# Optimization experiments

Hardware: AMD Instinct MI355X
Metric: run time of the kernel (lower is better)

The kernel has to match this reference:

```python
import jax, jax.numpy as jnp
import numpy as np

B, N, T, D, M, HOPS = 32, 300, 12, 64, 16, 2

def setup_inputs() -> dict:
    key = jax.random.key(0)
    ks = jax.random.split(key, 12)
    inp = {
        "X": jax.random.normal(ks[0], (B, D, N, T), dtype=jnp.float32),
        "timeEmbedding": jax.random.normal(ks[1], (B, N, T, D), dtype=jnp.float32),
        "adjW": jax.random.normal(ks[2], (N, D), dtype=jnp.float32) * (1.0 / np.sqrt(D)),
        "adjB": jnp.zeros((N,), dtype=jnp.float32),
        "trainW1": jax.random.normal(ks[3], (N, M), dtype=jnp.float32) * 0.1,
        "trainW2": jax.random.normal(ks[4], (M, D * D), dtype=jnp.float32) * 0.1,
        "alpha1": jax.random.normal(ks[5], (N, M), dtype=jnp.float32) * 0.1,
        "alpha2": jax.random.normal(ks[6], (M, N), dtype=jnp.float32) * 0.1,
        "beta1": jax.random.normal(ks[7], (N, M), dtype=jnp.float32) * 0.1,
        "beta2": jax.random.normal(ks[8], (M, N), dtype=jnp.float32) * 0.1,
        "gcnW": jax.random.normal(ks[9], (D, D * (HOPS + 1)), dtype=jnp.float32) * (1.0 / np.sqrt(D * (HOPS + 1))),
        "gcnB": jnp.zeros((D,), dtype=jnp.float32),
    }
    return inp

def reference(X, timeEmbedding, adjW, adjB, trainW1, trainW2, alpha1, alpha2, beta1, beta2, gcnW, gcnB):
    # timeEmbedding: [B,N,T,D] -> [B,T,N,D]
    te = jnp.transpose(timeEmbedding, (0, 2, 1, 3))
    # learned adjacency: A[b,t,n,k]
    A = jnp.sin(jnp.einsum('btnd,kd->btnk', te, adjW) + adjB)  # Linear(dmodel->N)
    A = (alpha1 @ alpha2) * A            # elementwise scale by [N,N], broadcast over b,t
    A = jax.nn.relu(A + beta1 @ beta2)
    # X: [B,D,N,T] -> [B,T,N,D]
    Xp = jnp.transpose(X, (0, 3, 2, 1))
    # per-node weight matrices [N,D,D]
    W = (trainW1 @ trainW2).reshape(N, D, D)
    Hs = [Xp]
    Hb = Xp
    for _ in range(HOPS):
        Hnow = jnp.einsum('btnk,btkd->btnd', A, Hb)      # adjacency aggregation
        Hnow = jnp.einsum('btnk,nkd->btnd', Hnow, W)     # per-node distinct matmul
        pre = Xp + Hnow
        Hnow = jax.nn.sigmoid(pre) * jnp.tanh(pre)        # gated residual
        Hs.append(Hnow)
        Hb = Hnow
    H = jnp.concatenate(Hs, axis=3)                       # [B,T,N,D*(hops+1)]
    Hout = jnp.einsum('btnf,df->btnd', H, gcnW) + gcnB    # gcnLinear (dropout = identity in eval)
    return jnp.transpose(Hout, (0, 3, 2, 1))              # [B,D,N,T]
```

## Files before the change

kernel.cpp:

```cpp
#include <hip/hip_runtime.h>

#define Nq 300
#define Tq 12
#define Dq 64
#define Mq 16
#define BTq 384
#define DDq (Dq*Dq)
#define Fq (Dq*3)
#define NP 320

typedef short bf8_t __attribute__((ext_vector_type(8)));
typedef float f4_t  __attribute__((ext_vector_type(4)));

__device__ __forceinline__ unsigned short f2bf(float f) {
    unsigned u = __float_as_uint(f);
    u = (u + 0x7FFFu + ((u >> 16) & 1u)) >> 16;
    return (unsigned short)u;
}
__device__ __forceinline__ float bf2f(unsigned short u) {
    return __uint_as_float((unsigned)u << 16);
}
__device__ __forceinline__ unsigned cvtpk(float lo, float hi) {
    unsigned r;
    asm("v_cvt_pk_bf16_f32 %0, %1, %2" : "=v"(r) : "v"(lo), "v"(hi));
    return r;
}
__device__ __forceinline__ float4 ld4(const float* p) { return *(const float4*)p; }

__device__ __forceinline__ bf8_t pack8(float4 a, float4 b) {
    union { unsigned u[4]; bf8_t v; } q;
    q.u[0] = cvtpk(a.x, a.y); q.u[1] = cvtpk(a.z, a.w);
    q.u[2] = cvtpk(b.x, b.y); q.u[3] = cvtpk(b.z, b.w);
    return q.v;
}

__device__ __forceinline__ float gatef(float p) {
    float pc = fminf(fmaxf(p, -30.f), 30.f);
    float u = __expf(pc);
    return u * (u - 1.f) / (u * u + 1.f);
}

__global__ void __launch_bounds__(256) kprep_all(
    const float* __restrict__ a1, const float* __restrict__ a2,
    const float* __restrict__ b1, const float* __restrict__ b2,
    const float* __restrict__ w1, const float* __restrict__ w2,
    const float* __restrict__ adjW, const float* __restrict__ adjB,
    const float* __restrict__ X,
    unsigned* __restrict__ ABt, unsigned short* __restrict__ Wt,
    unsigned short* __restrict__ adjWb, float* __restrict__ adjBp,
    unsigned short* __restrict__ Xp_t, unsigned short* __restrict__ Xp_nb)
{
    __shared__ char smem[64 * 308 * 2];
    const int vb = blockIdx.x;
    const int tid = threadIdx.x;

    if (vb < 400) {
        const int tile = vb;
        const int reg = tid & 3, lane = tid >> 2;
        const int nt = tile % 5;  int r1 = tile / 5;
        const int w  = r1 % 4;    int r2 = r1 / 4;
        const int c  = r2 % 5;    const int qi = r2 / 5;
        const int n = qi*80 + nt*16 + (lane & 15);
        const int k = c*64 + w*16 + (lane >> 4)*4 + reg;
        unsigned outv = 0u;
        if (n < Nq && k < Nq) {
            float sa = 0.f, sb = 0.f;
            #pragma unroll
            for (int m = 0; m < Mq; ++m) {
                sa = fmaf(a1[n*Mq+m], a2[m*Nq+k], sa);
                sb = fmaf(b1[n*Mq+m], b2[m*Nq+k], sb);
            }
            outv = cvtpk(sa, sb);
        }
        ABt[tile*256 + tid] = outv;
    } else if (vb < 700) {
        float* sT = (float*)smem;
        __shared__ float sw1[Mq];
        const int n = vb - 400;
        if (tid < Mq) sw1[tid] = w1[n*Mq + tid];
        __syncthreads();
        for (int i = tid; i < DDq; i += 256) {
            int k = i >> 6, d = i & 63;
            float s = 0.f;
            #pragma unroll
            for (int m = 0; m < Mq; ++m) s = fmaf(sw1[m], w2[m*DDq + i], s);
            sT[d*65 + k] = s;
        }
        __syncthreads();
        for (int i = tid; i < DDq; i += 256) {
            int d = i >> 6, k = i & 63;
            Wt[(size_t)n*DDq + i] = f2bf(sT[d*65 + k]);
        }
    } else if (vb < 780) {
        int e = (vb - 700) * 256 + tid;
        if (e < NP * 64) {
            int k = e >> 6, d = e & 63;
            adjWb[e] = (k < Nq) ? f2bf(adjW[k*Dq + d]) : (unsigned short)0;
        }
        if (e < NP) adjBp[e] = (e < Nq) ? adjB[e] : 0.f;
    } else {
        unsigned short* sT = (unsigned short*)smem;
        const int bx = vb - 780;
        const int b = bx / 24, sub = bx % 24;
        const int tile = sub >> 1, half = sub & 1;
        const int n0 = tile * 25, d0 = half * 32;
        for (int i = tid; i < 32 * 75; i += 256) {
            int dl = i / 75, jq = i - dl*75, j = jq*4;
            float4 v = ld4(&X[(size_t)(b*64 + d0 + dl)*3600 + n0*12 + j]);
            *(uint2*)&sT[dl*308 + j] = make_uint2(cvtpk(v.x, v.y), cvtpk(v.z, v.w));
        }
        __syncthreads();
        for (int wi = tid; wi < 12 * 32 * 25; wi += 256) {
            int nl = wi % 25, rem = wi / 25;
            int dl = rem & 31, t = rem >> 5;
            Xp_t[((size_t)(b*Tq + t)*64 + d0 + dl)*NP + n0 + nl] = sT[dl*308 + nl*12 + t];
        }
        if (tile == 11) {
            for (int wi = tid; wi < 12 * 32 * 20; wi += 256) {
                int e = wi % 20, rem = wi / 20;
                int dl = rem & 31, t = rem >> 5;
                Xp_t[((size_t)(b*Tq + t)*64 + d0 + dl)*NP + 300 + e] = 0;
            }
        }
        for (int wi = tid; wi < 25 * 12 * 8; wi += 256) {
            int dg = wi & 7, rem = wi >> 3;
            int t = rem % 12, nl = rem / 12;
            ushort4 o;
            o.x = sT[(dg*4+0)*308 + nl*12 + t];
            o.y = sT[(dg*4+1)*308 + nl*12 + t];
            o.z = sT[(dg*4+2)*308 + nl*12 + t];
            o.w = sT[(dg*4+3)*308 + nl*12 + t];
            *(ushort4*)&Xp_nb[((size_t)(n0+nl)*BTq + b*Tq + t)*64 + d0 + dg*4] = o;
        }
    }
}

__global__ void __launch_bounds__(256) ktr2(const unsigned short* __restrict__ Hnb,
                                            unsigned short* __restrict__ Ht) {
    __shared__ unsigned short sT[64 * 308];
    const int bt = blockIdx.x;
    const int tid = threadIdx.x;
    for (int i = tid; i < 300 * 8; i += 256) {
        int nl = i >> 3, dg = i & 7;
        bf8_t v = *(const bf8_t*)&Hnb[((size_t)nl*BTq + bt)*64 + dg*8];
        #pragma unroll
        for (int k = 0; k < 8; ++k)
            sT[(dg*8+k)*308 + nl] = (unsigned short)v[k];
    }
    __syncthreads();
    for (int wi = tid; wi < 64 * 80; wi += 256) {
        int kq = wi % 80, d = wi / 80;
        ushort4 o;
        int k = kq * 4;
        o.x = (k+0 < Nq) ? sT[d*308 + k+0] : (unsigned short)0;
        o.y = (k+1 < Nq) ? sT[d*308 + k+1] : (unsigned short)0;
        o.z = (k+2 < Nq) ? sT[d*308 + k+2] : (unsigned short)0;
        o.w = (k+3 < Nq) ? sT[d*308 + k+3] : (unsigned short)0;
        *(ushort4*)&Ht[((size_t)bt*64 + d)*NP + k] = o;
    }
}

template<int HOP>
__global__ void __launch_bounds__(256) kfuse_t(
    const float* __restrict__ te,
    unsigned short* __restrict__ teP,
    const unsigned short* __restrict__ adjWb,
    const float* __restrict__ adjBp,
    const unsigned* __restrict__ ABt,
    const unsigned short* __restrict__ Hb_t,
    unsigned short* __restrict__ Hout_nb)
{
    __shared__ unsigned short sP[80 * 72];
    __shared__ unsigned short sT[80 * 68];
    const int bt = blockIdx.x >> 2, qi = blockIdx.x & 3;
    const int b = bt / Tq, t = bt - b * Tq;
    const int nbase = qi * 80;
    const int tid = threadIdx.x;
    const int w = tid >> 6, lane = tid & 63, quad = lane >> 4, l16 = lane & 15;
    const int dcol = w*16 + l16;
    const int nrows = (Nq - nbase < 80) ? (Nq - nbase) : 80;

    if (HOP == 1) {
        #pragma unroll
        for (int r = 0; r < 5; ++r) {
            int row = r*16 + (tid >> 4);
            int col = (tid & 15) * 4;
            int n = nbase + row; if (n > Nq-1) n = Nq-1;
            float4 v = ld4(te + (((size_t)b*Nq + n)*Tq + t)*Dq + col);
            *(uint2*)&sT[row*68 + col] = make_uint2(cvtpk(v.x, v.y), cvtpk(v.z, v.w));
        }
    } else {
        for (int idx = tid; idx < 80*8; idx += 256) {
            int row = idx >> 3, cg = idx & 7;
            int n = nbase + row; if (n > Nq-1) n = Nq-1;
            *(bf8_t*)&sT[row*68 + cg*8] =
                *(const bf8_t*)&teP[((size_t)bt*Nq + n)*64 + cg*8];
        }
    }
    __syncthreads();
    if (HOP == 1) {
        for (int idx = tid; idx < nrows*8; idx += 256) {
            int row = idx >> 3, cg = idx & 7;
            *(bf8_t*)&teP[((size_t)bt*Nq + nbase + row)*64 + cg*8] =
                *(const bf8_t*)&sT[row*68 + cg*8];
        }
    }
    bf8_t tb0[5], tb1[5];
    #pragma unroll
    for (int nt = 0; nt < 5; ++nt) {
        const unsigned short* tr = &sT[(nt*16 + l16)*68];
        tb0[nt] = *(const bf8_t*)(tr + quad*8);
        tb1[nt] = *(const bf8_t*)(tr + 32 + quad*8);
    }

    f4_t accO[5];
    #pragma unroll
    for (int rt = 0; rt < 5; ++rt) accO[rt] = (f4_t){0.f, 0.f, 0.f, 0.f};

    const unsigned short* hr = Hb_t + ((size_t)bt*64 + dcol)*NP;

    for (int c = 0; c < 5; ++c) {
        const int cbase = c * 64;
        const unsigned* abbase = ABt + ((((size_t)qi*5 + c)*4 + w)*5)*256 + lane*4;
        uint4 abv[5];
        #pragma unroll
        for (int nt = 0; nt < 5; ++nt) abv[nt] = *(const uint4*)(abbase + nt*256);
        const unsigned short* ar = adjWb + (cbase + w*16 + l16)*64;
        bf8_t ka0 = *(const bf8_t*)(ar + quad*8);
        bf8_t ka1 = *(const bf8_t*)(ar + 32 + quad*8);
        float4 bias4 = ld4(adjBp + cbase + w*16 + quad*4);
        bf8_t hv0 = *(const bf8_t*)(hr + cbase + quad*8);
        bf8_t hv1 = *(const bf8_t*)(hr + cbase + 32 + quad*8);

        if (c > 0) __syncthreads();
        #pragma unroll
        for (int nt = 0; nt < 5; ++nt) {
            f4_t p = {0.f, 0.f, 0.f, 0.f};
            p = __builtin_amdgcn_mfma_f32_16x16x32_bf16(ka0, tb0[nt], p, 0, 0, 0);
            p = __builtin_amdgcn_mfma_f32_16x16x32_bf16(ka1, tb1[nt], p, 0, 0, 0);
            uint4 ab = abv[nt];
            float s0 = fmaxf(fmaf(__uint_as_float(ab.x << 16), __sinf(p[0] + bias4.x),
                                  __uint_as_float(ab.x & 0xFFFF0000u)), 0.f);
            float s1 = fmaxf(fmaf(__uint_as_float(ab.y << 16), __sinf(p[1] + bias4.y),
                                  __uint_as_float(ab.y & 0xFFFF0000u)), 0.f);
            float s2 = fmaxf(fmaf(__uint_as_float(ab.z << 16), __sinf(p[2] + bias4.z),
                                  __uint_as_float(ab.z & 0xFFFF0000u)), 0.f);
            float s3 = fmaxf(fmaf(__uint_as_float(ab.w << 16), __sinf(p[3] + bias4.w),
                                  __uint_as_float(ab.w & 0xFFFF0000u)), 0.f);
            *(uint2*)&sP[(nt*16 + l16)*72 + w*16 + quad*4] =
                make_uint2(cvtpk(s0, s1), cvtpk(s2, s3));
        }
        __syncthreads();
        #pragma unroll
        for (int rt = 0; rt < 5; ++rt) {
            bf8_t p0 = *(const bf8_t*)&sP[(rt*16 + l16)*72 + quad*8];
            bf8_t p1 = *(const bf8_t*)&sP[(rt*16 + l16)*72 + 32 + quad*8];
            accO[rt] = __builtin_amdgcn_mfma_f32_16x16x32_bf16(hv0, p0, accO[rt], 0, 0, 0);
            accO[rt] = __builtin_amdgcn_mfma_f32_16x16x32_bf16(hv1, p1, accO[rt], 0, 0, 0);
        }
    }
    #pragma unroll
    for (int rt = 0; rt < 5; ++rt) {
        *(uint2*)&sT[(rt*16 + l16)*68 + w*16 + quad*4] =
            make_uint2(cvtpk(accO[rt][0], accO[rt][1]),
                       cvtpk(accO[rt][2], accO[rt][3]));
    }
    __syncthreads();
    for (int idx = tid; idx < nrows*8; idx += 256) {
        int row = idx >> 3, cg = idx & 7;
        *(bf8_t*)&Hout_nb[((size_t)(nbase + row)*BTq + bt)*64 + cg*8] =
            *(const bf8_t*)&sT[row*68 + cg*8];
    }
}

__global__ void __launch_bounds__(256) kmm(
    const unsigned short* __restrict__ Hagg_nb,
    const unsigned short* __restrict__ Xp_nb,
    const unsigned short* __restrict__ Wt,
    unsigned short* __restrict__ Hout_nb)
{
    const int n = blockIdx.x >> 2, qi = blockIdx.x & 3;
    const int bt0 = qi * 96;
    const int tid = threadIdx.x;
    const int w = tid >> 6, lane = tid & 63, quad = lane >> 4, l16 = lane & 15;
    const int dcol = w*16 + l16;
    const unsigned short* wn = Wt + (size_t)n * DDq + dcol*64;
    bf8_t v0 = *(const bf8_t*)(wn + quad*8);
    bf8_t v1 = *(const bf8_t*)(wn + 32 + quad*8);
    bf8_t a0[6], a1[6];
    #pragma unroll
    for (int rt = 0; rt < 6; ++rt) {
        int r = bt0 + rt*16 + l16;
        const unsigned short* row = Hagg_nb + ((size_t)n*BTq + r)*64;
        a0[rt] = *(const bf8_t*)(row + quad*8);
        a1[rt] = *(const bf8_t*)(row + 32 + quad*8);
    }
    f4_t acc[6];
    #pragma unroll
    for (int rt = 0; rt < 6; ++rt) acc[rt] = (f4_t){0.f, 0.f, 0.f, 0.f};
    #pragma unroll
    for (int rt = 0; rt < 6; ++rt) {
        acc[rt] = __builtin_amdgcn_mfma_f32_16x16x32_bf16(v0, a0[rt], acc[rt], 0, 0, 0);
        acc[rt] = __builtin_amdgcn_mfma_f32_16x16x32_bf16(v1, a1[rt], acc[rt], 0, 0, 0);
    }
    __syncthreads();
    ushort4 xp4[6];
    #pragma unroll
    for (int rt = 0; rt < 6; ++rt) {
        int r = bt0 + rt*16 + l16;
        xp4[rt] = *(const ushort4*)&Xp_nb[((size_t)n*BTq + r)*64 + w*16 + quad*4];
    }
    #pragma unroll
    for (int rt = 0; rt < 6; ++rt) {
        int r = bt0 + rt*16 + l16;
        float g0 = gatef(bf2f(xp4[rt].x) + acc[rt][0]);
        float g1 = gatef(bf2f(xp4[rt].y) + acc[rt][1]);
        float g2 = gatef(bf2f(xp4[rt].z) + acc[rt][2]);
        float g3 = gatef(bf2f(xp4[rt].w) + acc[rt][3]);
        *(uint2*)&Hout_nb[((size_t)n*BTq + r)*64 + w*16 + quad*4] =
            make_uint2(cvtpk(g0, g1), cvtpk(g2, g3));
    }
}

__global__ void __launch_bounds__(256) kgcn(
    const unsigned short* __restrict__ Xp_nb, const unsigned short* __restrict__ H1_nb,
    const unsigned short* __restrict__ H2_nb, const float* __restrict__ gcnW,
    const float* __restrict__ gcnB, float* __restrict__ out)
{
    const int bid = blockIdx.x;
    const int b = bid / 57, rem = bid % 57;
    const int tile = rem / 3, rg = rem % 3;
    const int n0 = tile * 16;
    const int rows = (tile == 18) ? 144 : 192;
    const int r0base = rg * 64;
    const int tid = threadIdx.x;
    const int w = tid >> 6, lane = tid & 63, quad = lane >> 4, l16 = lane & 15;
    const int dcol = w*16 + l16;
    const float bias = gcnB[dcol];
    f4_t acc[4];
    #pragma unroll
    for (int rt = 0; rt < 4; ++rt) acc[rt] = (f4_t){0.f, 0.f, 0.f, 0.f};
    const unsigned short* bufs[3] = {Xp_nb, H1_nb, H2_nb};
    #pragma unroll
    for (int c = 0; c < 3; ++c) {
        const unsigned short* buf = bufs[c];
        const float* gwr = gcnW + (size_t)dcol*Fq + c*Dq;
        bf8_t v0 = pack8(ld4(gwr + quad*8),      ld4(gwr + quad*8 + 4));
        bf8_t v1 = pack8(ld4(gwr + 32 + quad*8), ld4(gwr + 36 + quad*8));
        #pragma unroll
        for (int rt = 0; rt < 4; ++rt) {
            int rr = r0base + rt*16;
            if (rr < rows) {
                int r = rr + l16;
                int nl = r / 12, t = r - nl*12;
                int n = n0 + nl; if (n > Nq-1) n = Nq-1;
                const unsigned short* row = buf + ((size_t)n*BTq + b*Tq + t)*64;
                bf8_t a0 = *(const bf8_t*)(row + quad*8);
                bf8_t a1 = *(const bf8_t*)(row + 32 + quad*8);
                acc[rt] = __builtin_amdgcn_mfma_f32_16x16x32_bf16(a0, v0, acc[rt], 0, 0, 0);
                acc[rt] = __builtin_amdgcn_mfma_f32_16x16x32_bf16(a1, v1, acc[rt], 0, 0, 0);
            }
        }
    }
    float* outd = out + (size_t)(b*Dq + dcol)*3600 + n0*12;
    #pragma unroll
    for (int rt = 0; rt < 4; ++rt) {
        int rr = r0base + rt*16;
        if (rr < rows) {
            int r0 = rr + quad*4;
            float4 o = make_float4(acc[rt][0] + bias, acc[rt][1] + bias,
                                   acc[rt][2] + bias, acc[rt][3] + bias);
            *(float4*)&outd[r0] = o;
        }
    }
}

extern "C" void kernel_launch(void* const* d_in, const int* in_sizes, int n_in,
                              void* d_out, int out_size, void* d_ws, size_t ws_size,
                              hipStream_t stream) {
    (void)in_sizes; (void)n_in; (void)out_size; (void)ws_size;
    const float* X    = (const float*)d_in[0];
    const float* te   = (const float*)d_in[1];
    const float* adjW = (const float*)d_in[2];
    const float* adjB = (const float*)d_in[3];
    const float* w1   = (const float*)d_in[4];
    const float* w2   = (const float*)d_in[5];
    const float* a1   = (const float*)d_in[6];
    const float* a2   = (const float*)d_in[7];
    const float* b1   = (const float*)d_in[8];
    const float* b2   = (const float*)d_in[9];
    const float* gW   = (const float*)d_in[10];
    const float* gB   = (const float*)d_in[11];
    float* out = (float*)d_out;

    char* ws = (char*)d_ws;
    unsigned*       ABt    = (unsigned*)      (ws);
    unsigned short* adjWb  = (unsigned short*)(ws + 409600);
    float*          adjBp  = (float*)         (ws + 450560);
    unsigned short* Wt     = (unsigned short*)(ws + 451840);
    unsigned short* Xp_t   = (unsigned short*)(ws + 2909440);
    unsigned short* Xp_nb  = (unsigned short*)(ws + 18638080);
    unsigned short* Hagg   = (unsigned short*)(ws + 33383680);
    unsigned short* H1_nb  = (unsigned short*)(ws + 48129280);
    unsigned short* H1_t   = (unsigned short*)(ws + 62874880);
    unsigned short* teP    = (unsigned short*)(ws + 78603520);

    hipLaunchKernelGGL(kprep_all, dim3(1548), dim3(256), 0, stream,
                       a1, a2, b1, b2, w1, w2, adjW, adjB, X,
                       ABt, Wt, adjWb, adjBp, Xp_t, Xp_nb);
    hipLaunchKernelGGL(HIP_KERNEL_NAME(kfuse_t<1>), dim3(1536), dim3(256), 0, stream,
                       te, teP, adjWb, adjBp, ABt, Xp_t, Hagg);
    hipLaunchKernelGGL(kmm,   dim3(1200), dim3(256), 0, stream, Hagg, Xp_nb, Wt, H1_nb);
    hipLaunchKernelGGL(ktr2,  dim3(384),  dim3(256), 0, stream, H1_nb, H1_t);
    hipLaunchKernelGGL(HIP_KERNEL_NAME(kfuse_t<2>), dim3(1536), dim3(256), 0, stream,
                       te, teP, adjWb, adjBp, ABt, H1_t, Hagg);
    hipLaunchKernelGGL(kmm,   dim3(1200), dim3(256), 0, stream, Hagg, Xp_nb, Wt, Hagg);
    hipLaunchKernelGGL(kgcn,  dim3(1824), dim3(256), 0, stream, Xp_nb, H1_nb, Hagg, gW, gB, out);
}
```

Baseline: 288.9 us.

## Stage gcn inputs and outputs through LDS and vectorize X transpose stores

The X transpose in the prep kernel now processes 12-node tiles across all 64 channels, writing Xp_t with 4-wide and Xp_nb with 8-wide vector stores instead of scalar and 4-wide ones. The gcn kernel now stages each 192-row input tile into LDS with coalesced 16-byte loads and buffers results in LDS. It then writes contiguous float4 rows to the [B,D,N,T] output, replacing strided direct stores. This targets uncoalesced global accesses, at the cost of extra LDS traffic, more barriers and fewer gcn blocks.

```diff
diff --git a/kernel.cpp b/kernel.cpp
--- a/kernel.cpp
+++ b/kernel.cpp
@@ -50,7 +50,7 @@
     unsigned short* __restrict__ adjWb, float* __restrict__ adjBp,
     unsigned short* __restrict__ Xp_t, unsigned short* __restrict__ Xp_nb)
 {
-    __shared__ char smem[64 * 308 * 2];
+    __shared__ __align__(16) char smem[64 * 308 * 2];
     const int vb = blockIdx.x;
     const int tid = threadIdx.x;
 
@@ -101,36 +101,39 @@
     } else {
         unsigned short* sT = (unsigned short*)smem;
         const int bx = vb - 780;
-        const int b = bx / 24, sub = bx % 24;
-        const int tile = sub >> 1, half = sub & 1;
-        const int n0 = tile * 25, d0 = half * 32;
-        for (int i = tid; i < 32 * 75; i += 256) {
-            int dl = i / 75, jq = i - dl*75, j = jq*4;
-            float4 v = ld4(&X[(size_t)(b*64 + d0 + dl)*3600 + n0*12 + j]);
-            *(uint2*)&sT[dl*308 + j] = make_uint2(cvtpk(v.x, v.y), cvtpk(v.z, v.w));
+        const int b = bx / 25, tile = bx % 25;
+        const int n0 = tile * 12;
+        for (int wi = tid; wi < 64 * 36; wi += 256) {
+            int jq = wi % 36, dl = wi / 36;
+            float4 v = ld4(&X[(size_t)(b*64 + dl)*3600 + n0*12 + jq*4]);
+            *(uint2*)&sT[dl*152 + jq*4] = make_uint2(cvtpk(v.x, v.y), cvtpk(v.z, v.w));
         }
         __syncthreads();
-        for (int wi = tid; wi < 12 * 32 * 25; wi += 256) {
-            int nl = wi % 25, rem = wi / 25;
-            int dl = rem & 31, t = rem >> 5;
-            Xp_t[((size_t)(b*Tq + t)*64 + d0 + dl)*NP + n0 + nl] = sT[dl*308 + nl*12 + t];
-        }
-        if (tile == 11) {
-            for (int wi = tid; wi < 12 * 32 * 20; wi += 256) {
-                int e = wi % 20, rem = wi / 20;
-                int dl = rem & 31, t = rem >> 5;
-                Xp_t[((size_t)(b*Tq + t)*64 + d0 + dl)*NP + 300 + e] = 0;
+        for (int wi = tid; wi < 12 * 64 * 3; wi += 256) {
+            int cg = wi % 3, rem = wi / 3;
+            int d = rem & 63, t = rem >> 6;
+            ushort4 o;
+            o.x = sT[d*152 + (cg*4+0)*12 + t];
+            o.y = sT[d*152 + (cg*4+1)*12 + t];
+            o.z = sT[d*152 + (cg*4+2)*12 + t];
+            o.w = sT[d*152 + (cg*4+3)*12 + t];
+            *(ushort4*)&Xp_t[((size_t)(b*Tq + t)*64 + d)*NP + n0 + cg*4] = o;
+        }
+        if (tile == 24) {
+            for (int wi = tid; wi < 12 * 64 * 5; wi += 256) {
+                int cg = wi % 5, rem = wi / 5;
+                int d = rem & 63, t = rem >> 6;
+                ushort4 z; z.x = 0; z.y = 0; z.z = 0; z.w = 0;
+                *(ushort4*)&Xp_t[((size_t)(b*Tq + t)*64 + d)*NP + 300 + cg*4] = z;
             }
         }
-        for (int wi = tid; wi < 25 * 12 * 8; wi += 256) {
+        for (int wi = tid; wi < 12 * 12 * 8; wi += 256) {
             int dg = wi & 7, rem = wi >> 3;
             int t = rem % 12, nl = rem / 12;
-            ushort4 o;
-            o.x = sT[(dg*4+0)*308 + nl*12 + t];
-            o.y = sT[(dg*4+1)*308 + nl*12 + t];
-            o.z = sT[(dg*4+2)*308 + nl*12 + t];
-            o.w = sT[(dg*4+3)*308 + nl*12 + t];
-            *(ushort4*)&Xp_nb[((size_t)(n0+nl)*BTq + b*Tq + t)*64 + d0 + dg*4] = o;
+            union { unsigned short s[8]; bf8_t v; } o;
+            #pragma unroll
+            for (int k = 0; k < 8; ++k) o.s[k] = sT[(dg*8+k)*152 + nl*12 + t];
+            *(bf8_t*)&Xp_nb[((size_t)(n0+nl)*BTq + b*Tq + t)*64 + dg*8] = o.v;
         }
     }
 }
@@ -327,51 +330,65 @@
     const unsigned short* __restrict__ H2_nb, const float* __restrict__ gcnW,
     const float* __restrict__ gcnB, float* __restrict__ out)
 {
+    __shared__ __align__(16) char smem[16 * 816 * 2];
+    unsigned short* sBuf = (unsigned short*)smem;
+    float* sOut = (float*)smem;
     const int bid = blockIdx.x;
-    const int b = bid / 57, rem = bid % 57;
-    const int tile = rem / 3, rg = rem % 3;
+    const int b = bid / 38, rem2 = bid % 38;
+    const int tile = rem2 >> 1, dh = rem2 & 1;
     const int n0 = tile * 16;
     const int rows = (tile == 18) ? 144 : 192;
-    const int r0base = rg * 64;
+    const int bt0 = b * Tq;
     const int tid = threadIdx.x;
     const int w = tid >> 6, lane = tid & 63, quad = lane >> 4, l16 = lane & 15;
-    const int dcol = w*16 + l16;
+    const int wd = w & 1, wr = w >> 1;
+    const int dcol = dh*32 + wd*16 + l16;
     const float bias = gcnB[dcol];
-    f4_t acc[4];
-    #pragma unroll
-    for (int rt = 0; rt < 4; ++rt) acc[rt] = (f4_t){0.f, 0.f, 0.f, 0.f};
+    f4_t acc[6];
+    #pragma unroll
+    for (int rt = 0; rt < 6; ++rt) acc[rt] = (f4_t){0.f, 0.f, 0.f, 0.f};
     const unsigned short* bufs[3] = {Xp_nb, H1_nb, H2_nb};
-    #pragma unroll
     for (int c = 0; c < 3; ++c) {
-        const unsigned short* buf = bufs[c];
         const float* gwr = gcnW + (size_t)dcol*Fq + c*Dq;
         bf8_t v0 = pack8(ld4(gwr + quad*8),      ld4(gwr + quad*8 + 4));
         bf8_t v1 = pack8(ld4(gwr + 32 + quad*8), ld4(gwr + 36 + quad*8));
-        #pragma unroll
-        for (int rt = 0; rt < 4; ++rt) {
-            int rr = r0base + rt*16;
-            if (rr < rows) {
-                int r = rr + l16;
-                int nl = r / 12, t = r - nl*12;
-                int n = n0 + nl; if (n > Nq-1) n = Nq-1;
-                const unsigned short* row = buf + ((size_t)n*BTq + b*Tq + t)*64;
-                bf8_t a0 = *(const bf8_t*)(row + quad*8);
-                bf8_t a1 = *(const bf8_t*)(row + 32 + quad*8);
-                acc[rt] = __builtin_amdgcn_mfma_f32_16x16x32_bf16(a0, v0, acc[rt], 0, 0, 0);
-                acc[rt] = __builtin_amdgcn_mfma_f32_16x16x32_bf16(a1, v1, acc[rt], 0, 0, 0);
-            }
-        }
-    }
-    float* outd = out + (size_t)(b*Dq + dcol)*3600 + n0*12;
-    #pragma unroll
-    for (int rt = 0; rt < 4; ++rt) {
-        int rr = r0base + rt*16;
-        if (rr < rows) {
-            int r0 = rr + quad*4;
-            float4 o = make_float4(acc[rt][0] + bias, acc[rt][1] + bias,
-                                   acc[rt][2] + bias, acc[rt][3] + bias);
-            *(float4*)&outd[r0] = o;
-        }
+        const unsigned short* buf = bufs[c];
+        if (c > 0) __syncthreads();
+        for (int wi = tid; wi < 16*12*8; wi += 256) {
+            int cg = wi & 7, rem = wi >> 3;
+            int t = rem % 12, nl = rem / 12;
+            int n = n0 + nl; if (n > Nq-1) n = Nq-1;
+            *(bf8_t*)&sBuf[(nl*12 + t)*68 + cg*8] =
+                *(const bf8_t*)&buf[((size_t)n*BTq + bt0 + t)*64 + cg*8];
+        }
+        __syncthreads();
+        #pragma unroll
+        for (int rt = 0; rt < 6; ++rt) {
+            int r = (wr*6 + rt)*16 + l16;
+            const unsigned short* row = &sBuf[r*68];
+            bf8_t a0 = *(const bf8_t*)(row + quad*8);
+            bf8_t a1 = *(const bf8_t*)(row + 32 + quad*8);
+            acc[rt] = __builtin_amdgcn_mfma_f32_16x16x32_bf16(a0, v0, acc[rt], 0, 0, 0);
+            acc[rt] = __builtin_amdgcn_mfma_f32_16x16x32_bf16(a1, v1, acc[rt], 0, 0, 0);
+        }
+    }
+    __syncthreads();
+    const int dl = wd*16 + l16;
+    #pragma unroll
+    for (int rt = 0; rt < 6; ++rt) {
+        int rr = (wr*6 + rt)*16;
+        float4 o = make_float4(acc[rt][0] + bias, acc[rt][1] + bias,
+                               acc[rt][2] + bias, acc[rt][3] + bias);
+        *(float4*)&sOut[dl*196 + rr + quad*4] = o;
+    }
+    __syncthreads();
+    float* outb = out + (size_t)(b*Dq + dh*32)*3600 + n0*12;
+    const int f4max = rows >> 2;
+    for (int wi = tid; wi < 32*48; wi += 256) {
+        int f4i = wi % 48, dli = wi / 48;
+        if (f4i < f4max)
+            *(float4*)&outb[(size_t)dli*3600 + f4i*4] =
+                *(const float4*)&sOut[dli*196 + f4i*4];
     }
 }
 
@@ -405,7 +422,7 @@
     unsigned short* H1_t   = (unsigned short*)(ws + 62874880);
     unsigned short* teP    = (unsigned short*)(ws + 78603520);
 
-    hipLaunchKernelGGL(kprep_all, dim3(1548), dim3(256), 0, stream,
+    hipLaunchKernelGGL(kprep_all, dim3(1580), dim3(256), 0, stream,
                        a1, a2, b1, b2, w1, w2, adjW, adjB, X,
                        ABt, Wt, adjWb, adjBp, Xp_t, Xp_nb);
     hipLaunchKernelGGL(HIP_KERNEL_NAME(kfuse_t<1>), dim3(1536), dim3(256), 0, stream,
@@ -415,5 +432,5 @@
     hipLaunchKernelGGL(HIP_KERNEL_NAME(kfuse_t<2>), dim3(1536), dim3(256), 0, stream,
                        te, teP, adjWb, adjBp, ABt, H1_t, Hagg);
     hipLaunchKernelGGL(kmm,   dim3(1200), dim3(256), 0, stream, Hagg, Xp_nb, Wt, Hagg);
-    hipLaunchKernelGGL(kgcn,  dim3(1824), dim3(256), 0, stream, Xp_nb, H1_nb, Hagg, gW, gB, out);
-}
+    hipLaunchKernelGGL(kgcn,  dim3(1216), dim3(256), 0, stream, Xp_nb, H1_nb, Hagg, gW, gB, out);
+}
```

Result: no change. 285.0 us (-1.3%).
